# Performance work log

Hardware: AMD Instinct MI355X
Metric: run time of the kernel (lower is better)

Reference implementation:

```python
import jax, jax.numpy as jnp
import numpy as np

SIGMA = 4.0
KSIZE = 2 * int(4.0 * SIGMA + 0.5) + 1  # 33, as in anomalib's GaussianBlur2d
INPUT_SIZE = (224, 224)
NUM_NEIGHBORS = 9


def avg_pool_4_1_1(x):
    # nn.AvgPool2d(kernel_size=4, stride=1, padding=1), count_include_pad=True -> divide by 16
    s = jax.lax.reduce_window(x, 0.0, jax.lax.add, (1, 1, 4, 4), (1, 1, 1, 1),
                              ((0, 0), (0, 0), (1, 1), (1, 1)))
    return s / 16.0


def gaussian_kernel1d(ksize, sigma):
    x = jnp.arange(ksize, dtype=jnp.float32) - (ksize - 1) / 2.0
    g = jnp.exp(-0.5 * (x / sigma) ** 2)
    return g / jnp.sum(g)


def gaussian_blur(x):
    # separable 33x33 gaussian blur, reflect padding (kornia GaussianBlur2d default)
    k = gaussian_kernel1d(KSIZE, SIGMA)
    pad = KSIZE // 2
    xp = jnp.pad(x, ((0, 0), (0, 0), (pad, pad), (pad, pad)), mode='reflect')
    dn = ('NCHW', 'OIHW', 'NCHW')
    y = jax.lax.conv_general_dilated(xp, k.reshape(1, 1, KSIZE, 1), (1, 1), 'VALID', dimension_numbers=dn)
    y = jax.lax.conv_general_dilated(y, k.reshape(1, 1, 1, KSIZE), (1, 1), 'VALID', dimension_numbers=dn)
    return y


def euclidean_dist(x, y):
    # pairwise L2: x [..., n, d], y [..., m, d] -> [..., n, m]
    x2 = jnp.sum(x * x, axis=-1, keepdims=True)
    y2 = jnp.sum(y * y, axis=-1, keepdims=True)
    d2 = x2 - 2.0 * jnp.matmul(x, jnp.swapaxes(y, -1, -2)) + jnp.swapaxes(y2, -1, -2)
    return jnp.sqrt(jnp.clip(d2, 0.0, None))


def compute_anomaly_score(patch_scores, locations, embedding, memory_bank):
    # PatchCore re-weighting (num_neighbors > 1 branch)
    B, P = patch_scores.shape
    bidx = jnp.arange(B)
    max_patches = jnp.argmax(patch_scores, axis=1)                      # [B]
    feats = embedding.reshape(B, P, -1)[bidx, max_patches]              # [B, C]
    score = patch_scores[bidx, max_patches]                             # [B] s*
    nn_index = locations[bidx, max_patches]                             # [B]
    nn_sample = memory_bank[nn_index]                                   # [B, C]
    d_bank = euclidean_dist(nn_sample, memory_bank)                     # [B, M]
    _, support = jax.lax.top_k(-d_bank, NUM_NEIGHBORS)                  # [B, K] smallest
    support_feats = memory_bank[support]                                # [B, K, C]
    distances = euclidean_dist(feats[:, None, :], support_feats)        # [B, 1, K]
    weights = 1.0 - jnp.exp(score) / jnp.sum(jnp.exp(distances[:, 0, :]), axis=-1)
    return weights * score


def setup_inputs() -> dict:
    key = jax.random.key(0)
    k1, k2, k3 = jax.random.split(key, 3)
    feat_layer2 = jax.random.normal(k1, (8, 512, 28, 28), dtype=jnp.float32)
    feat_layer3 = jax.random.normal(k2, (8, 1024, 14, 14), dtype=jnp.float32)
    memory_bank = jax.random.normal(k3, (32000, 1536), dtype=jnp.float32)
    return {"feat_layer2": feat_layer2, "feat_layer3": feat_layer3, "memory_bank": memory_bank}


def reference(feat_layer2, feat_layer3, memory_bank):
    # feature_pooler = AvgPool2d(4,1,1)
    f2 = avg_pool_4_1_1(feat_layer2)   # [B, 512, 27, 27]
    f3 = avg_pool_4_1_1(feat_layer3)   # [B, 1024, 13, 13]
    B, _, H, W = f2.shape
    # generate_embedding: bilinear upsample layer3 to layer2 size, concat channels
    f3u = jax.image.resize(f3, (B, f3.shape[1], H, W), method='bilinear')
    emb = jnp.concatenate([f2, f3u], axis=1)                            # [B, 1536, 27, 27]
    C = emb.shape[1]
    embedding = jnp.transpose(emb, (0, 2, 3, 1)).reshape(-1, C)         # [B*H*W, C]
    # nearest_neighbors with n_neighbors=1 over the coreset memory bank
    d = euclidean_dist(embedding, memory_bank)                          # [B*H*W, M]
    patch_scores = jnp.min(d, axis=1).reshape(B, -1)
    locations = jnp.argmin(d, axis=1).reshape(B, -1)
    pred_score = compute_anomaly_score(patch_scores, locations, embedding, memory_bank)
    # anomaly map: upsample patch scores to input size + gaussian blur
    pmap = patch_scores.reshape(B, 1, H, W)
    amap = jax.image.resize(pmap, (B, 1, INPUT_SIZE[0], INPUT_SIZE[1]), method='bilinear')
    anomaly_map = gaussian_blur(amap)
    return anomaly_map, pred_score
```

## Files before the change

kernel.cpp:

```cpp
#include <hip/hip_runtime.h>
#include <math.h>

#define NB 8
#define C2 512
#define C3 1024
#define HIN2 28
#define HIN3 14
#define HO2 27
#define HO3 13
#define CC 1536
#define NP (NB*HO2*HO2)
#define NM 32000
#define NKNN 9
#define OH 224
#define AMAP_N (NB*OH*OH)

#define BM 256
#define BN 256
#define BK 64
#define KT (CC/BK)
#define MB_CNT ((NP+BM-1)/BM)
#define NB_CNT (NM/BN)
#define NWG (MB_CNT*NB_CNT)

typedef unsigned long long u64;
typedef unsigned int u32;
typedef __attribute__((ext_vector_type(8))) short bf16x8;
typedef __attribute__((ext_vector_type(4))) float f32x4;

struct GW { float w[33]; };

__device__ __forceinline__ float warp_sum(float v){
  #pragma unroll
  for (int off=32; off; off>>=1) v += __shfl_down(v, off);
  return v;
}

__device__ __forceinline__ ushort f2bf(float f){
  u32 u = __float_as_uint(f);
  u32 r = (u + 0x7FFFu + ((u>>16)&1u)) >> 16;
  return (ushort)r;
}
__device__ __forceinline__ float bf2f(ushort b){
  return __uint_as_float(((u32)b)<<16);
}

#define GLDS(g, l) __builtin_amdgcn_global_load_lds((const __attribute__((address_space(1))) void*)(g), (__attribute__((address_space(3))) void*)(l), 16, 0, 0)
#define WAITVM2() asm volatile("s_waitcnt vmcnt(2)" ::: "memory")
#define WAITVM0() asm volatile("s_waitcnt vmcnt(0)" ::: "memory")
__device__ __forceinline__ void bar_raw(){
  asm volatile("" ::: "memory");
  __builtin_amdgcn_s_barrier();
  asm volatile("" ::: "memory");
}

__global__ void k_avgpool2(const float* __restrict__ in, ushort* __restrict__ embB){
  int t = blockIdx.x*256 + threadIdx.x;
  if (t >= NB*HO2*HO2*C2) return;
  int c = t % C2; int r = t / C2;
  int j = r % HO2; r /= HO2;
  int i = r % HO2; int b = r / HO2;
  const float* plane = in + ((size_t)(b*C2 + c)*HIN2)*HIN2;
  float s = 0.f;
  #pragma unroll
  for (int di=0; di<4; ++di){
    int y = i - 1 + di;
    if ((unsigned)y >= HIN2) continue;
    #pragma unroll
    for (int dj=0; dj<4; ++dj){
      int x = j - 1 + dj;
      if ((unsigned)x < HIN2) s += plane[y*HIN2 + x];
    }
  }
  embB[((size_t)((b*HO2 + i)*HO2 + j))*CC + c] = f2bf(s * (1.f/16.f));
}

__global__ void k_avgpool3(const float* __restrict__ in, float* __restrict__ f3p){
  int t = blockIdx.x*256 + threadIdx.x;
  if (t >= NB*HO3*HO3*C3) return;
  int c = t % C3; int r = t / C3;
  int j = r % HO3; r /= HO3;
  int i = r % HO3; int b = r / HO3;
  const float* plane = in + ((size_t)(b*C3 + c)*HIN3)*HIN3;
  float s = 0.f;
  #pragma unroll
  for (int di=0; di<4; ++di){
    int y = i - 1 + di;
    if ((unsigned)y >= HIN3) continue;
    #pragma unroll
    for (int dj=0; dj<4; ++dj){
      int x = j - 1 + dj;
      if ((unsigned)x < HIN3) s += plane[y*HIN3 + x];
    }
  }
  f3p[((size_t)((b*HO3 + i)*HO3 + j))*C3 + c] = s * (1.f/16.f);
}

__global__ void k_upsample3(const float* __restrict__ f3p, ushort* __restrict__ embB){
  int t = blockIdx.x*256 + threadIdx.x;
  if (t >= NB*HO2*HO2*C3) return;
  int c = t % C3; int r = t / C3;
  int ox = r % HO2; r /= HO2;
  int oy = r % HO2; int b = r / HO2;
  float fy = (oy + 0.5f) * (13.f/27.f) - 0.5f;
  float fx = (ox + 0.5f) * (13.f/27.f) - 0.5f;
  int y0 = (int)floorf(fy); float wy = fy - (float)y0;
  int x0 = (int)floorf(fx); float wx = fx - (float)x0;
  int y0c = min(max(y0,0), HO3-1), y1c = min(max(y0+1,0), HO3-1);
  int x0c = min(max(x0,0), HO3-1), x1c = min(max(x0+1,0), HO3-1);
  const float* base = f3p + (size_t)(b*HO3*HO3)*C3;
  float v00 = base[(size_t)(y0c*HO3 + x0c)*C3 + c];
  float v01 = base[(size_t)(y0c*HO3 + x1c)*C3 + c];
  float v10 = base[(size_t)(y1c*HO3 + x0c)*C3 + c];
  float v11 = base[(size_t)(y1c*HO3 + x1c)*C3 + c];
  float v = (1.f-wy)*((1.f-wx)*v00 + wx*v01) + wy*((1.f-wx)*v10 + wx*v11);
  embB[((size_t)((b*HO2 + oy)*HO2 + ox))*CC + C2 + c] = f2bf(v);
}

__global__ void k_bank_prep(const float* __restrict__ bank, ushort* __restrict__ bankB,
                            float* __restrict__ y2){
  int wave = threadIdx.x >> 6, lane = threadIdx.x & 63;
  int r = blockIdx.x*4 + wave;
  if (r >= NM) return;
  const float4* p = (const float4*)(bank + (size_t)r*CC);
  ushort4* q = (ushort4*)(bankB + (size_t)r*CC);
  float s = 0.f;
  #pragma unroll
  for (int it=0; it<6; ++it){
    float4 v = p[it*64 + lane];
    s += v.x*v.x + v.y*v.y + v.z*v.z + v.w*v.w;
    ushort4 o; o.x = f2bf(v.x); o.y = f2bf(v.y); o.z = f2bf(v.z); o.w = f2bf(v.w);
    q[it*64 + lane] = o;
  }
  s = warp_sum(s);
  if (lane==0) y2[r] = s;
}

__global__ void k_rowsumsq_bf(const ushort* __restrict__ src, float* __restrict__ dst, int rows){
  int wave = threadIdx.x >> 6;
  int lane = threadIdx.x & 63;
  int r = blockIdx.x*4 + wave;
  if (r >= rows) return;
  const uint4* p = (const uint4*)(src + (size_t)r*CC);
  float s = 0.f;
  #pragma unroll
  for (int it=0; it<3; ++it){
    uint4 v = p[it*64 + lane];
    u32 ws_[4] = {v.x, v.y, v.z, v.w};
    #pragma unroll
    for (int q=0;q<4;q++){
      float lo = __uint_as_float(ws_[q]<<16);
      float hi = __uint_as_float(ws_[q]&0xFFFF0000u);
      s += lo*lo + hi*hi;
    }
  }
  s = warp_sum(s);
  if (lane==0) dst[r] = s;
}

__global__ void k_init(u64* __restrict__ packed){
  int t = blockIdx.x*256 + threadIdx.x;
  if (t < NP) packed[t] = ~0ull;
}

__global__ __launch_bounds__(512, 2) void k_distmin_mfma(
    const ushort* __restrict__ A, const ushort* __restrict__ B,
    const float* __restrict__ x2, const float* __restrict__ y2,
    u64* __restrict__ packed)
{
  __shared__ ushort smem[4*BM*BK];
  ushort* As0 = smem;
  ushort* Bs0 = smem + BM*BK;
  ushort* As1 = smem + 2*BM*BK;
  ushort* Bs1 = smem + 3*BM*BK;

  const int tid = threadIdx.x;
  const int w   = tid >> 6;
  const int l   = tid & 63;
  const int wr  = w >> 2;
  const int wc  = w & 3;
  const int ccol = l & 15;
  const int cgrp = l >> 4;

  int orig = blockIdx.x;
  const int q8 = NWG/8, r8 = NWG%8;
  int xcd = orig & 7, sidx = orig >> 3;
  int wg = (xcd < r8 ? xcd*(q8+1) : r8*(q8+1) + (xcd-r8)*q8) + sidx;
  const int mb = wg % MB_CNT;
  const int nb = wg / MB_CNT;
  const int m0 = mb * BM;
  const int n0 = nb * BN;

  const int rowin = l >> 3;
  const int scol  = (((l&7) ^ rowin) * 8);
  int chA1[2], chA2[2], chB1[2], chB2[2];
  u32 aO1[2], aO2[2], bO1[2], bO2[2];
  u32 lA1[2], lA2[2], lB1[2], lB2[2];
  #pragma unroll
  for (int c=0;c<2;c++){
    chA1[c] = (w<4) ? (2*w+c) : (8+2*w+c);
    chA2[c] = chA1[c] + 8;
    chB1[c] = (w>>1)*8 + (w&1)*2 + c;
    chB2[c] = chB1[c] + 4;
    aO1[c] = (u32)min(m0 + chA1[c]*8 + rowin, NP-1)*CC + scol;
    aO2[c] = (u32)min(m0 + chA2[c]*8 + rowin, NP-1)*CC + scol;
    bO1[c] = (u32)(n0 + chB1[c]*8 + rowin)*CC + scol;
    bO2[c] = (u32)(n0 + chB2[c]*8 + rowin)*CC + scol;
    lA1[c] = (u32)chA1[c]*1024 + l*16;
    lA2[c] = (u32)chA2[c]*1024 + l*16;
    lB1[c] = (u32)chB1[c]*1024 + l*16;
    lB2[c] = (u32)chB2[c]*1024 + l*16;
  }

  const u32 o0 = (u32)((cgrp ^ (ccol & 7)) * 8);
  u32 aRow[8], bRow[4];
  #pragma unroll
  for (int mi=0;mi<8;mi++) aRow[mi] = (u32)(wr*128 + mi*16 + ccol)*BK;
  #pragma unroll
  for (int ni=0;ni<4;ni++) bRow[ni] = (u32)(wc*64 + ni*16 + ccol)*BK;

  f32x4 acc[8][4];
  #pragma unroll
  for (int mi=0;mi<8;mi++)
    #pragma unroll
    for (int ni=0;ni<4;ni++)
      acc[mi][ni] = (f32x4){0.f,0.f,0.f,0.f};

  bf16x8 rAlo[4][2], rAhi[4][2], rBlo[2][2], rBhi[2][2];

  #pragma unroll
  for (int c=0;c<2;c++) GLDS(A + aO1[c], (char*)As0 + lA1[c]);
  #pragma unroll
  for (int c=0;c<2;c++) GLDS(B + bO1[c], (char*)Bs0 + lB1[c]);
  WAITVM0(); bar_raw();
  #pragma unroll
  for (int mi=0;mi<4;mi++)
    #pragma unroll
    for (int ks=0;ks<2;ks++)
      rAlo[mi][ks] = *(const bf16x8*)&As0[aRow[mi] + (o0 ^ (u32)(ks<<5))];
  #pragma unroll
  for (int ni=0;ni<2;ni++)
    #pragma unroll
    for (int ks=0;ks<2;ks++)
      rBlo[ni][ks] = *(const bf16x8*)&Bs0[bRow[ni] + (o0 ^ (u32)(ks<<5))];
  #pragma unroll
  for (int c=0;c<2;c++) GLDS(B + bO2[c], (char*)Bs0 + lB2[c]);
  #pragma unroll
  for (int c=0;c<2;c++) GLDS(A + aO2[c], (char*)As0 + lA2[c]);

  const ushort* cA = As0; const ushort* cB = Bs0;
  ushort* nA = As1; ushort* nB = Bs1;

  #pragma unroll 1
  for (int kt=0; kt<KT; ++kt){
    const u32 kk = (u32)(kt+1)*BK;

    WAITVM2(); bar_raw(); __builtin_amdgcn_sched_barrier(0);
    GLDS(A + aO1[0] + kk, (char*)nA + lA1[0]);
    GLDS(A + aO1[1] + kk, (char*)nA + lA1[1]);
    #pragma unroll
    for (int ni=0;ni<2;ni++)
      #pragma unroll
      for (int ks=0;ks<2;ks++)
        rBhi[ni][ks] = *(const bf16x8*)&cB[bRow[ni+2] + (o0 ^ (u32)(ks<<5))];
    __builtin_amdgcn_s_setprio(1);
    #pragma unroll
    for (int mi=0;mi<4;mi++)
      #pragma unroll
      for (int ni=0;ni<2;ni++)
        #pragma unroll
        for (int ks=0;ks<2;ks++)
          acc[mi][ni] = __builtin_amdgcn_mfma_f32_16x16x32_bf16(rAlo[mi][ks], rBlo[ni][ks], acc[mi][ni], 0, 0, 0);
    __builtin_amdgcn_s_setprio(0);

    WAITVM2(); bar_raw(); __builtin_amdgcn_sched_barrier(0);
    GLDS(B + bO1[0] + kk, (char*)nB + lB1[0]);
    GLDS(B + bO1[1] + kk, (char*)nB + lB1[1]);
    #pragma unroll
    for (int mi=0;mi<4;mi++)
      #pragma unroll
      for (int ks=0;ks<2;ks++)
        rAhi[mi][ks] = *(const bf16x8*)&cA[aRow[mi+4] + (o0 ^ (u32)(ks<<5))];
    __builtin_amdgcn_s_setprio(1);
    #pragma unroll
    for (int mi=0;mi<4;mi++)
      #pragma unroll
      for (int ni=0;ni<2;ni++)
        #pragma unroll
        for (int ks=0;ks<2;ks++)
          acc[mi][ni+2] = __builtin_amdgcn_mfma_f32_16x16x32_bf16(rAlo[mi][ks], rBhi[ni][ks], acc[mi][ni+2], 0, 0, 0);
    __builtin_amdgcn_s_setprio(0);

    WAITVM2(); bar_raw(); __builtin_amdgcn_sched_barrier(0);
    GLDS(B + bO2[0] + kk, (char*)nB + lB2[0]);
    GLDS(B + bO2[1] + kk, (char*)nB + lB2[1]);
    #pragma unroll
    for (int mi=0;mi<4;mi++)
      #pragma unroll
      for (int ks=0;ks<2;ks++)
        rAlo[mi][ks] = *(const bf16x8*)&((const ushort*)nA)[aRow[mi] + (o0 ^ (u32)(ks<<5))];
    __builtin_amdgcn_s_setprio(1);
    #pragma unroll
    for (int mi=0;mi<4;mi++)
      #pragma unroll
      for (int ni=0;ni<2;ni++)
        #pragma unroll
        for (int ks=0;ks<2;ks++)
          acc[mi+4][ni] = __builtin_amdgcn_mfma_f32_16x16x32_bf16(rAhi[mi][ks], rBlo[ni][ks], acc[mi+4][ni], 0, 0, 0);
    __builtin_amdgcn_s_setprio(0);

    WAITVM2(); bar_raw(); __builtin_amdgcn_sched_barrier(0);
    GLDS(A + aO2[0] + kk, (char*)nA + lA2[0]);
    GLDS(A + aO2[1] + kk, (char*)nA + lA2[1]);
    #pragma unroll
    for (int ni=0;ni<2;ni++)
      #pragma unroll
      for (int ks=0;ks<2;ks++)
        rBlo[ni][ks] = *(const bf16x8*)&((const ushort*)nB)[bRow[ni] + (o0 ^ (u32)(ks<<5))];
    __builtin_amdgcn_s_setprio(1);
    #pragma unroll
    for (int mi=0;mi<4;mi++)
      #pragma unroll
      for (int ni=0;ni<2;ni++)
        #pragma unroll
        for (int ks=0;ks<2;ks++)
          acc[mi+4][ni+2] = __builtin_amdgcn_mfma_f32_16x16x32_bf16(rAhi[mi][ks], rBhi[ni][ks], acc[mi+4][ni+2], 0, 0, 0);
    __builtin_amdgcn_s_setprio(0);

    ushort* t1 = (ushort*)cA; cA = nA; nA = t1;
    ushort* t2 = (ushort*)cB; cB = nB; nB = t2;
  }
  WAITVM0();

  float xv[8][4];
  #pragma unroll
  for (int mi=0;mi<8;mi++)
    #pragma unroll
    for (int r=0;r<4;r++)
      xv[mi][r] = x2[min(m0 + wr*128 + mi*16 + cgrp*4 + r, NP-1)];

  u64 best[8][4];
  #pragma unroll
  for (int mi=0;mi<8;mi++)
    #pragma unroll
    for (int r=0;r<4;r++) best[mi][r] = ~0ull;

  #pragma unroll
  for (int ni=0;ni<4;ni++){
    const int n = n0 + wc*64 + ni*16 + ccol;
    const float yy = y2[n];
    #pragma unroll
    for (int mi=0;mi<8;mi++)
      #pragma unroll
      for (int r=0;r<4;r++){
        float d2 = fmaxf(xv[mi][r] + yy - 2.f*acc[mi][ni][r], 0.f);
        u64 pk = (((u64)__float_as_uint(d2))<<32) | (u32)n;
        if (pk < best[mi][r]) best[mi][r] = pk;
      }
  }

  #pragma unroll
  for (int mi=0;mi<8;mi++)
    #pragma unroll
    for (int r=0;r<4;r++){
      u64 pk = best[mi][r];
      #pragma unroll
      for (int md=1; md<16; md<<=1){
        u64 o = __shfl_xor(pk, md);
        if (o < pk) pk = o;
      }
      const int row = m0 + wr*128 + mi*16 + cgrp*4 + r;
      if (ccol==0 && row < NP) atomicMin(&packed[row], pk);
    }
}

__global__ void k_unpack(const u64* __restrict__ packed, float* __restrict__ patch_d, int* __restrict__ loc){
  int t = blockIdx.x*256 + threadIdx.x;
  if (t < NP){
    u64 v = packed[t];
    patch_d[t] = sqrtf(__uint_as_float((u32)(v>>32)));
    loc[t] = (int)(v & 0xffffffffu);
  }
}

__global__ void k_argmax(const float* __restrict__ patch_d, const int* __restrict__ loc,
                         int* __restrict__ sel_mp, float* __restrict__ sel_score, int* __restrict__ sel_nn){
  int b = blockIdx.x;
  int tid = threadIdx.x;
  __shared__ u64 red[4];
  u64 best = 0;
  for (int p = tid; p < HO2*HO2; p += 256){
    float v = patch_d[b*HO2*HO2 + p];
    u64 pk = (((u64)__float_as_uint(v))<<32) | (u32)(HO2*HO2 - p);
    if (pk > best) best = pk;
  }
  int lane = tid & 63, w = tid >> 6;
  #pragma unroll
  for (int d=32; d; d>>=1){ u64 o = __shfl_down(best, d); if (o > best) best = o; }
  if (lane==0) red[w] = best;
  __syncthreads();
  if (tid==0){
    u64 bb = red[0];
    for (int q=1;q<4;q++) if (red[q] > bb) bb = red[q];
    int p = HO2*HO2 - (int)(bb & 0xffffffffu);
    sel_mp[b] = p;
    sel_score[b] = __uint_as_float((u32)(bb>>32));
    sel_nn[b] = loc[b*HO2*HO2 + p];
  }
}

__device__ __forceinline__ void bf8dec(uint4 v, float* f){
  u32 a[4] = {v.x, v.y, v.z, v.w};
  #pragma unroll
  for (int q=0;q<4;q++){
    f[2*q]   = __uint_as_float(a[q]<<16);
    f[2*q+1] = __uint_as_float(a[q]&0xFFFF0000u);
  }
}

__global__ __launch_bounds__(256) void k_dbank(const ushort* __restrict__ bankB, const float* __restrict__ y2,
    const int* __restrict__ sel_nn, float* __restrict__ d_bank){
  int wave = threadIdx.x >> 6, lane = threadIdx.x & 63;
  int m = blockIdx.x*4 + wave;
  if (m >= NM) return;
  int nn[NB];
  #pragma unroll
  for (int b=0;b<NB;b++) nn[b] = sel_nn[b];
  const uint4* pm = (const uint4*)(bankB + (size_t)m*CC);
  float acc[NB];
  #pragma unroll
  for (int b=0;b<NB;b++) acc[b] = 0.f;
  #pragma unroll
  for (int it=0; it<3; ++it){
    uint4 v = pm[it*64 + lane];
    float vf[8]; bf8dec(v, vf);
    #pragma unroll
    for (int b=0;b<NB;b++){
      uint4 u = ((const uint4*)(bankB + (size_t)nn[b]*CC))[it*64 + lane];
      float uf[8]; bf8dec(u, uf);
      #pragma unroll
      for (int q=0;q<8;q++) acc[b] += vf[q]*uf[q];
    }
  }
  #pragma unroll
  for (int b=0;b<NB;b++){
    float s = warp_sum(acc[b]);
    if (lane==0) d_bank[(size_t)b*NM + m] = fmaxf(y2[nn[b]] + y2[m] - 2.f*s, 0.f);
  }
}

__global__ __launch_bounds__(256) void k_score(const float* __restrict__ d_bank, const float* __restrict__ bank,
    const ushort* __restrict__ embB, const float* __restrict__ x2, const float* __restrict__ y2,
    const int* __restrict__ sel_mp, const float* __restrict__ sel_score, float* __restrict__ out_score){
  int b = blockIdx.x, tid = threadIdx.x;
  __shared__ u64 cand[256*NKNN];
  __shared__ int sel[NKNN];
  __shared__ u64 red[4];
  __shared__ u64 gbest_s;
  __shared__ float fred[4];
  __shared__ float sumexp_s;

  #pragma unroll
  for (int q=0;q<NKNN;q++) cand[tid*NKNN+q] = ~0ull;
  for (int m = tid; m < NM; m += 256){
    float v = d_bank[(size_t)b*NM + m];
    u64 pk = (((u64)__float_as_uint(v))<<32) | (u32)m;
    if (pk < cand[tid*NKNN + NKNN-1]){
      cand[tid*NKNN + NKNN-1] = pk;
      for (int q=NKNN-1; q>0 && cand[tid*NKNN+q] < cand[tid*NKNN+q-1]; --q){
        u64 t = cand[tid*NKNN+q]; cand[tid*NKNN+q] = cand[tid*NKNN+q-1]; cand[tid*NKNN+q-1] = t;
      }
    }
  }
  __syncthreads();
  int lane = tid & 63, w = tid >> 6;
  for (int k=0;k<NKNN;++k){
    u64 mybest = ~0ull;
    #pragma unroll
    for (int q=0;q<NKNN;q++){ u64 v = cand[tid*NKNN+q]; if (v < mybest) mybest = v; }
    u64 rb = mybest;
    #pragma unroll
    for (int d=32; d; d>>=1){ u64 o = __shfl_down(rb, d); if (o < rb) rb = o; }
    if (lane==0) red[w] = rb;
    __syncthreads();
    if (tid==0){
      u64 bb = red[0];
      for (int q=1;q<4;q++) if (red[q] < bb) bb = red[q];
      gbest_s = bb;
      sel[k] = (int)(bb & 0xffffffffu);
    }
    __syncthreads();
    u64 gb = gbest_s;
    #pragma unroll
    for (int q=0;q<NKNN;q++) if (cand[tid*NKNN+q] == gb) cand[tid*NKNN+q] = ~0ull;
    __syncthreads();
  }

  int mp = sel_mp[b];
  const ushort* fv = embB + (size_t)(b*HO2*HO2 + mp)*CC;
  float fx2 = x2[b*HO2*HO2 + mp];
  if (tid==0) sumexp_s = 0.f;
  __syncthreads();
  for (int k=0;k<NKNN;++k){
    const float* sv = bank + (size_t)sel[k]*CC;
    float part = 0.f;
    for (int i = tid; i < CC; i += 256) part += bf2f(fv[i])*sv[i];
    part = warp_sum(part);
    if (lane==0) fred[w] = part;
    __syncthreads();
    if (tid==0){
      float dot = fred[0]+fred[1]+fred[2]+fred[3];
      float d2 = fmaxf(fx2 + y2[sel[k]] - 2.f*dot, 0.f);
      sumexp_s += expf(sqrtf(d2));
    }
    __syncthreads();
  }
  if (tid==0){
    float s = sel_score[b];
    out_score[b] = (1.f - expf(s)/sumexp_s) * s;
  }
}

__global__ void k_amap_bilinear(const float* __restrict__ patch_d, float* __restrict__ amap){
  int t = blockIdx.x*256 + threadIdx.x;
  if (t >= AMAP_N) return;
  int x = t % OH; int r = t / OH;
  int y = r % OH; int b = r / OH;
  float fy = (y + 0.5f) * (27.f/224.f) - 0.5f;
  float fx = (x + 0.5f) * (27.f/224.f) - 0.5f;
  int y0 = (int)floorf(fy); float wy = fy - (float)y0;
  int x0 = (int)floorf(fx); float wx = fx - (float)x0;
  int y0c = min(max(y0,0),HO2-1), y1c = min(max(y0+1,0),HO2-1);
  int x0c = min(max(x0,0),HO2-1), x1c = min(max(x0+1,0),HO2-1);
  const float* p = patch_d + b*HO2*HO2;
  float v = (1.f-wy)*((1.f-wx)*p[y0c*HO2+x0c] + wx*p[y0c*HO2+x1c])
          + wy*((1.f-wx)*p[y1c*HO2+x0c] + wx*p[y1c*HO2+x1c]);
  amap[t] = v;
}

__global__ void k_blur_h(const float* __restrict__ in, float* __restrict__ out, GW gw){
  int t = blockIdx.x*256 + threadIdx.x;
  if (t >= AMAP_N) return;
  int x = t % OH; int rest = t / OH;
  const float* row = in + (size_t)rest*OH;
  float s = 0.f;
  #pragma unroll
  for (int k=0;k<33;++k){
    int xx = x + k - 16;
    xx = (xx < 0) ? -xx : xx;
    xx = (xx > OH-1) ? (2*(OH-1) - xx) : xx;
    s += gw.w[k]*row[xx];
  }
  out[t] = s;
}

__global__ void k_blur_v(const float* __restrict__ in, float* __restrict__ out, GW gw){
  int t = blockIdx.x*256 + threadIdx.x;
  if (t >= AMAP_N) return;
  int x = t % OH; int r = t / OH;
  int y = r % OH; int b = r / OH;
  const float* img = in + (size_t)b*OH*OH;
  float s = 0.f;
  #pragma unroll
  for (int k=0;k<33;++k){
    int yy = y + k - 16;
    yy = (yy < 0) ? -yy : yy;
    yy = (yy > OH-1) ? (2*(OH-1) - yy) : yy;
    s += gw.w[k]*img[(size_t)yy*OH + x];
  }
  out[t] = s;
}

extern "C" void kernel_launch(void* const* d_in, const int* in_sizes, int n_in,
                              void* d_out, int out_size, void* d_ws, size_t ws_size,
                              hipStream_t stream){
  const float* f2   = (const float*)d_in[0];
  const float* f3   = (const float*)d_in[1];
  const float* bank = (const float*)d_in[2];
  float* out = (float*)d_out;

  char* ws = (char*)d_ws;
  size_t off = 0;
  auto alloc = [&](size_t bytes)->char*{ char* p = ws + off; off += (bytes + 255) & ~(size_t)255; return p; };
  ushort* embB    = (ushort*)alloc((size_t)NP*CC*2);
  ushort* bankB   = (ushort*)alloc((size_t)NM*CC*2);
  float* f3p      = (float*)alloc((size_t)NB*HO3*HO3*C3*4);
  float* y2       = (float*)alloc((size_t)NM*4);
  float* x2       = (float*)alloc((size_t)NP*4);
  u64*   packed   = (u64*)  alloc((size_t)NP*8);
  float* patch_d  = (float*)alloc((size_t)NP*4);
  int*   loc      = (int*)  alloc((size_t)NP*4);
  float* d_bank   = (float*)alloc((size_t)NB*NM*4);
  int*   sel_mp   = (int*)  alloc(NB*4);
  float* sel_scr  = (float*)alloc(NB*4);
  int*   sel_nn   = (int*)  alloc(NB*4);
  float* amap1    = (float*)alloc((size_t)AMAP_N*4);
  float* amap2    = (float*)alloc((size_t)AMAP_N*4);

  GW gw;
  { float s=0.f; for(int i=0;i<33;i++){ float xx=(float)i-16.f; gw.w[i]=expf(-0.5f*(xx/4.f)*(xx/4.f)); s+=gw.w[i]; }
    for(int i=0;i<33;i++) gw.w[i]/=s; }

  k_avgpool2<<<(NB*HO2*HO2*C2+255)/256,256,0,stream>>>(f2, embB);
  k_avgpool3<<<(NB*HO3*HO3*C3+255)/256,256,0,stream>>>(f3, f3p);
  k_upsample3<<<(NB*HO2*HO2*C3+255)/256,256,0,stream>>>(f3p, embB);
  k_bank_prep<<<(NM+3)/4,256,0,stream>>>(bank, bankB, y2);
  k_rowsumsq_bf<<<(NP+3)/4,256,0,stream>>>(embB, x2, NP);
  k_init<<<(NP+255)/256,256,0,stream>>>(packed);
  k_distmin_mfma<<<NWG,512,0,stream>>>(embB, bankB, x2, y2, packed);
  k_unpack<<<(NP+255)/256,256,0,stream>>>(packed, patch_d, loc);
  k_argmax<<<NB,256,0,stream>>>(patch_d, loc, sel_mp, sel_scr, sel_nn);
  k_dbank<<<(NM+3)/4,256,0,stream>>>(bankB, y2, sel_nn, d_bank);
  k_score<<<NB,256,0,stream>>>(d_bank, bank, embB, x2, y2, sel_mp, sel_scr, out + AMAP_N);
  k_amap_bilinear<<<(AMAP_N+255)/256,256,0,stream>>>(patch_d, amap1);
  k_blur_h<<<(AMAP_N+255)/256,256,0,stream>>>(amap1, amap2, gw);
  k_blur_v<<<(AMAP_N+255)/256,256,0,stream>>>(amap2, out, gw);
}
```

Measured before the change: 1.041 ms.

## Restructure GEMM pipeline, stage avgpool in LDS, fuse upsample+blur as matrix

Reworks the MFMA distance-min main loop so each quarter reads its LDS fragments from the current buffer right before use, with vmcnt(4) waits and extra barriers, instead of prefetching from the next buffer. The avgpool kernels now stage per-channel planes in shared memory with coalesced float4 loads, and the packed-init is folded into the row-norm kernel. The bilinear upsample and separable reflect blur are folded into one precomputed 224x27 operator applied as two small matmuls per image in a single kernel. k_score moves to 512 threads. The extra barriers in the GEMM could add stalls, and the fused anomaly-map kernel runs only 8 blocks.

```diff
diff --git a/kernel.cpp b/kernel.cpp
--- a/kernel.cpp
+++ b/kernel.cpp
@@ -46,54 +46,74 @@
 }
 
 #define GLDS(g, l) __builtin_amdgcn_global_load_lds((const __attribute__((address_space(1))) void*)(g), (__attribute__((address_space(3))) void*)(l), 16, 0, 0)
-#define WAITVM2() asm volatile("s_waitcnt vmcnt(2)" ::: "memory")
+#define WAITVM4() asm volatile("s_waitcnt vmcnt(4)" ::: "memory")
 #define WAITVM0() asm volatile("s_waitcnt vmcnt(0)" ::: "memory")
+#define WAITLGKM0() asm volatile("s_waitcnt lgkmcnt(0)" ::: "memory")
+#define SB0() __builtin_amdgcn_sched_barrier(0)
 __device__ __forceinline__ void bar_raw(){
   asm volatile("" ::: "memory");
   __builtin_amdgcn_s_barrier();
   asm volatile("" ::: "memory");
 }
 
-__global__ void k_avgpool2(const float* __restrict__ in, ushort* __restrict__ embB){
-  int t = blockIdx.x*256 + threadIdx.x;
-  if (t >= NB*HO2*HO2*C2) return;
-  int c = t % C2; int r = t / C2;
-  int j = r % HO2; r /= HO2;
-  int i = r % HO2; int b = r / HO2;
-  const float* plane = in + ((size_t)(b*C2 + c)*HIN2)*HIN2;
-  float s = 0.f;
-  #pragma unroll
-  for (int di=0; di<4; ++di){
-    int y = i - 1 + di;
-    if ((unsigned)y >= HIN2) continue;
-    #pragma unroll
-    for (int dj=0; dj<4; ++dj){
-      int x = j - 1 + dj;
-      if ((unsigned)x < HIN2) s += plane[y*HIN2 + x];
-    }
-  }
-  embB[((size_t)((b*HO2 + i)*HO2 + j))*CC + c] = f2bf(s * (1.f/16.f));
-}
-
-__global__ void k_avgpool3(const float* __restrict__ in, float* __restrict__ f3p){
-  int t = blockIdx.x*256 + threadIdx.x;
-  if (t >= NB*HO3*HO3*C3) return;
-  int c = t % C3; int r = t / C3;
-  int j = r % HO3; r /= HO3;
-  int i = r % HO3; int b = r / HO3;
-  const float* plane = in + ((size_t)(b*C3 + c)*HIN3)*HIN3;
-  float s = 0.f;
-  #pragma unroll
-  for (int di=0; di<4; ++di){
-    int y = i - 1 + di;
-    if ((unsigned)y >= HIN3) continue;
-    #pragma unroll
-    for (int dj=0; dj<4; ++dj){
-      int x = j - 1 + dj;
-      if ((unsigned)x < HIN3) s += plane[y*HIN3 + x];
-    }
-  }
-  f3p[((size_t)((b*HO3 + i)*HO3 + j))*C3 + c] = s * (1.f/16.f);
+__global__ __launch_bounds__(256) void k_avgpool2(const float* __restrict__ in, ushort* __restrict__ embB){
+  __shared__ float pl[16*789];
+  int b = blockIdx.x >> 5, cg = blockIdx.x & 31;
+  const float4* src = (const float4*)(in + ((size_t)b*C2 + cg*16)*(HIN2*HIN2));
+  for (int idx = threadIdx.x; idx < 16*196; idx += 256){
+    int c = idx/196, p4 = idx - c*196;
+    float4 v = src[idx];
+    float* d = &pl[c*789 + p4*4];
+    d[0]=v.x; d[1]=v.y; d[2]=v.z; d[3]=v.w;
+  }
+  __syncthreads();
+  int c = threadIdx.x & 15, g = threadIdx.x >> 4;
+  for (int pos = g; pos < HO2*HO2; pos += 16){
+    int i = pos/HO2, j = pos - i*HO2;
+    const float* p = &pl[c*789];
+    float s = 0.f;
+    #pragma unroll
+    for (int di=0; di<4; ++di){
+      int y = i - 1 + di;
+      if ((unsigned)y >= HIN2) continue;
+      #pragma unroll
+      for (int dj=0; dj<4; ++dj){
+        int x = j - 1 + dj;
+        if ((unsigned)x < HIN2) s += p[y*HIN2 + x];
+      }
+    }
+    embB[((size_t)((b*HO2 + i)*HO2 + j))*CC + cg*16 + c] = f2bf(s * (1.f/16.f));
+  }
+}
+
+__global__ __launch_bounds__(256) void k_avgpool3(const float* __restrict__ in, float* __restrict__ f3p){
+  __shared__ float pl[64*197];
+  int b = blockIdx.x >> 4, cg = blockIdx.x & 15;
+  const float4* src = (const float4*)(in + ((size_t)b*C3 + cg*64)*(HIN3*HIN3));
+  for (int idx = threadIdx.x; idx < 64*49; idx += 256){
+    int c = idx/49, p4 = idx - c*49;
+    float4 v = src[idx];
+    float* d = &pl[c*197 + p4*4];
+    d[0]=v.x; d[1]=v.y; d[2]=v.z; d[3]=v.w;
+  }
+  __syncthreads();
+  int c = threadIdx.x & 63, g = threadIdx.x >> 6;
+  for (int pos = g; pos < HO3*HO3; pos += 4){
+    int i = pos/HO3, j = pos - i*HO3;
+    const float* p = &pl[c*197];
+    float s = 0.f;
+    #pragma unroll
+    for (int di=0; di<4; ++di){
+      int y = i - 1 + di;
+      if ((unsigned)y >= HIN3) continue;
+      #pragma unroll
+      for (int dj=0; dj<4; ++dj){
+        int x = j - 1 + dj;
+        if ((unsigned)x < HIN3) s += p[y*HIN3 + x];
+      }
+    }
+    f3p[((size_t)((b*HO3 + i)*HO3 + j))*C3 + cg*64 + c] = s * (1.f/16.f);
+  }
 }
 
 __global__ void k_upsample3(const float* __restrict__ f3p, ushort* __restrict__ embB){
@@ -136,7 +156,8 @@
   if (lane==0) y2[r] = s;
 }
 
-__global__ void k_rowsumsq_bf(const ushort* __restrict__ src, float* __restrict__ dst, int rows){
+__global__ void k_rowsumsq_bf(const ushort* __restrict__ src, float* __restrict__ dst, int rows,
+                              u64* __restrict__ packed){
   int wave = threadIdx.x >> 6;
   int lane = threadIdx.x & 63;
   int r = blockIdx.x*4 + wave;
@@ -155,12 +176,7 @@
     }
   }
   s = warp_sum(s);
-  if (lane==0) dst[r] = s;
-}
-
-__global__ void k_init(u64* __restrict__ packed){
-  int t = blockIdx.x*256 + threadIdx.x;
-  if (t < NP) packed[t] = ~0ull;
+  if (lane==0){ dst[r] = s; packed[r] = ~0ull; }
 }
 
 __global__ __launch_bounds__(512, 2) void k_distmin_mfma(
@@ -228,25 +244,16 @@
 
   bf16x8 rAlo[4][2], rAhi[4][2], rBlo[2][2], rBhi[2][2];
 
-  #pragma unroll
-  for (int c=0;c<2;c++) GLDS(A + aO1[c], (char*)As0 + lA1[c]);
-  #pragma unroll
-  for (int c=0;c<2;c++) GLDS(B + bO1[c], (char*)Bs0 + lB1[c]);
-  WAITVM0(); bar_raw();
-  #pragma unroll
-  for (int mi=0;mi<4;mi++)
-    #pragma unroll
-    for (int ks=0;ks<2;ks++)
-      rAlo[mi][ks] = *(const bf16x8*)&As0[aRow[mi] + (o0 ^ (u32)(ks<<5))];
-  #pragma unroll
-  for (int ni=0;ni<2;ni++)
-    #pragma unroll
-    for (int ks=0;ks<2;ks++)
-      rBlo[ni][ks] = *(const bf16x8*)&Bs0[bRow[ni] + (o0 ^ (u32)(ks<<5))];
-  #pragma unroll
-  for (int c=0;c<2;c++) GLDS(B + bO2[c], (char*)Bs0 + lB2[c]);
-  #pragma unroll
-  for (int c=0;c<2;c++) GLDS(A + aO2[c], (char*)As0 + lA2[c]);
+  GLDS(A + aO1[0], (char*)As0 + lA1[0]);
+  GLDS(A + aO1[1], (char*)As0 + lA1[1]);
+  GLDS(B + bO1[0], (char*)Bs0 + lB1[0]);
+  GLDS(B + bO1[1], (char*)Bs0 + lB1[1]);
+  GLDS(B + bO2[0], (char*)Bs0 + lB2[0]);
+  GLDS(B + bO2[1], (char*)Bs0 + lB2[1]);
+  GLDS(A + aO2[0], (char*)As0 + lA2[0]);
+  GLDS(A + aO2[1], (char*)As0 + lA2[1]);
+  WAITVM4();
+  bar_raw();
 
   const ushort* cA = As0; const ushort* cB = Bs0;
   ushort* nA = As1; ushort* nB = Bs1;
@@ -255,14 +262,19 @@
   for (int kt=0; kt<KT; ++kt){
     const u32 kk = (u32)(kt+1)*BK;
 
-    WAITVM2(); bar_raw(); __builtin_amdgcn_sched_barrier(0);
+    #pragma unroll
+    for (int mi=0;mi<4;mi++)
+      #pragma unroll
+      for (int ks=0;ks<2;ks++)
+        rAlo[mi][ks] = *(const bf16x8*)&cA[aRow[mi] + (o0 ^ (u32)(ks<<5))];
+    #pragma unroll
+    for (int ni=0;ni<2;ni++)
+      #pragma unroll
+      for (int ks=0;ks<2;ks++)
+        rBlo[ni][ks] = *(const bf16x8*)&cB[bRow[ni] + (o0 ^ (u32)(ks<<5))];
     GLDS(A + aO1[0] + kk, (char*)nA + lA1[0]);
     GLDS(A + aO1[1] + kk, (char*)nA + lA1[1]);
-    #pragma unroll
-    for (int ni=0;ni<2;ni++)
-      #pragma unroll
-      for (int ks=0;ks<2;ks++)
-        rBhi[ni][ks] = *(const bf16x8*)&cB[bRow[ni+2] + (o0 ^ (u32)(ks<<5))];
+    bar_raw(); WAITLGKM0(); SB0();
     __builtin_amdgcn_s_setprio(1);
     #pragma unroll
     for (int mi=0;mi<4;mi++)
@@ -272,15 +284,17 @@
         for (int ks=0;ks<2;ks++)
           acc[mi][ni] = __builtin_amdgcn_mfma_f32_16x16x32_bf16(rAlo[mi][ks], rBlo[ni][ks], acc[mi][ni], 0, 0, 0);
     __builtin_amdgcn_s_setprio(0);
-
-    WAITVM2(); bar_raw(); __builtin_amdgcn_sched_barrier(0);
+    WAITVM4();
+    bar_raw();
+
+    #pragma unroll
+    for (int ni=0;ni<2;ni++)
+      #pragma unroll
+      for (int ks=0;ks<2;ks++)
+        rBhi[ni][ks] = *(const bf16x8*)&cB[bRow[ni+2] + (o0 ^ (u32)(ks<<5))];
     GLDS(B + bO1[0] + kk, (char*)nB + lB1[0]);
     GLDS(B + bO1[1] + kk, (char*)nB + lB1[1]);
-    #pragma unroll
-    for (int mi=0;mi<4;mi++)
-      #pragma unroll
-      for (int ks=0;ks<2;ks++)
-        rAhi[mi][ks] = *(const bf16x8*)&cA[aRow[mi+4] + (o0 ^ (u32)(ks<<5))];
+    bar_raw(); WAITLGKM0(); SB0();
     __builtin_amdgcn_s_setprio(1);
     #pragma unroll
     for (int mi=0;mi<4;mi++)
@@ -290,15 +304,17 @@
         for (int ks=0;ks<2;ks++)
           acc[mi][ni+2] = __builtin_amdgcn_mfma_f32_16x16x32_bf16(rAlo[mi][ks], rBhi[ni][ks], acc[mi][ni+2], 0, 0, 0);
     __builtin_amdgcn_s_setprio(0);
-
-    WAITVM2(); bar_raw(); __builtin_amdgcn_sched_barrier(0);
+    WAITVM4();
+    bar_raw();
+
+    #pragma unroll
+    for (int mi=0;mi<4;mi++)
+      #pragma unroll
+      for (int ks=0;ks<2;ks++)
+        rAhi[mi][ks] = *(const bf16x8*)&cA[aRow[mi+4] + (o0 ^ (u32)(ks<<5))];
     GLDS(B + bO2[0] + kk, (char*)nB + lB2[0]);
     GLDS(B + bO2[1] + kk, (char*)nB + lB2[1]);
-    #pragma unroll
-    for (int mi=0;mi<4;mi++)
-      #pragma unroll
-      for (int ks=0;ks<2;ks++)
-        rAlo[mi][ks] = *(const bf16x8*)&((const ushort*)nA)[aRow[mi] + (o0 ^ (u32)(ks<<5))];
+    bar_raw(); WAITLGKM0(); SB0();
     __builtin_amdgcn_s_setprio(1);
     #pragma unroll
     for (int mi=0;mi<4;mi++)
@@ -308,15 +324,11 @@
         for (int ks=0;ks<2;ks++)
           acc[mi+4][ni] = __builtin_amdgcn_mfma_f32_16x16x32_bf16(rAhi[mi][ks], rBlo[ni][ks], acc[mi+4][ni], 0, 0, 0);
     __builtin_amdgcn_s_setprio(0);
-
-    WAITVM2(); bar_raw(); __builtin_amdgcn_sched_barrier(0);
+    bar_raw();
+
     GLDS(A + aO2[0] + kk, (char*)nA + lA2[0]);
     GLDS(A + aO2[1] + kk, (char*)nA + lA2[1]);
-    #pragma unroll
-    for (int ni=0;ni<2;ni++)
-      #pragma unroll
-      for (int ks=0;ks<2;ks++)
-        rBlo[ni][ks] = *(const bf16x8*)&((const ushort*)nB)[bRow[ni] + (o0 ^ (u32)(ks<<5))];
+    bar_raw();
     __builtin_amdgcn_s_setprio(1);
     #pragma unroll
     for (int mi=0;mi<4;mi++)
@@ -326,6 +338,8 @@
         for (int ks=0;ks<2;ks++)
           acc[mi+4][ni+2] = __builtin_amdgcn_mfma_f32_16x16x32_bf16(rAhi[mi][ks], rBhi[ni][ks], acc[mi+4][ni+2], 0, 0, 0);
     __builtin_amdgcn_s_setprio(0);
+    WAITVM4();
+    bar_raw();
 
     ushort* t1 = (ushort*)cA; cA = nA; nA = t1;
     ushort* t2 = (ushort*)cB; cB = nB; nB = t2;
@@ -449,20 +463,20 @@
   }
 }
 
-__global__ __launch_bounds__(256) void k_score(const float* __restrict__ d_bank, const float* __restrict__ bank,
+__global__ __launch_bounds__(512) void k_score(const float* __restrict__ d_bank, const float* __restrict__ bank,
     const ushort* __restrict__ embB, const float* __restrict__ x2, const float* __restrict__ y2,
     const int* __restrict__ sel_mp, const float* __restrict__ sel_score, float* __restrict__ out_score){
   int b = blockIdx.x, tid = threadIdx.x;
-  __shared__ u64 cand[256*NKNN];
+  __shared__ u64 cand[512*NKNN];
   __shared__ int sel[NKNN];
-  __shared__ u64 red[4];
+  __shared__ u64 red[8];
   __shared__ u64 gbest_s;
-  __shared__ float fred[4];
+  __shared__ float fred[8];
   __shared__ float sumexp_s;
 
   #pragma unroll
   for (int q=0;q<NKNN;q++) cand[tid*NKNN+q] = ~0ull;
-  for (int m = tid; m < NM; m += 256){
+  for (int m = tid; m < NM; m += 512){
     float v = d_bank[(size_t)b*NM + m];
     u64 pk = (((u64)__float_as_uint(v))<<32) | (u32)m;
     if (pk < cand[tid*NKNN + NKNN-1]){
@@ -485,7 +499,7 @@
     __syncthreads();
     if (tid==0){
       u64 bb = red[0];
-      for (int q=1;q<4;q++) if (red[q] < bb) bb = red[q];
+      for (int q=1;q<8;q++) if (red[q] < bb) bb = red[q];
       gbest_s = bb;
       sel[k] = (int)(bb & 0xffffffffu);
     }
@@ -504,12 +518,13 @@
   for (int k=0;k<NKNN;++k){
     const float* sv = bank + (size_t)sel[k]*CC;
     float part = 0.f;
-    for (int i = tid; i < CC; i += 256) part += bf2f(fv[i])*sv[i];
+    for (int i = tid; i < CC; i += 512) part += bf2f(fv[i])*sv[i];
     part = warp_sum(part);
     if (lane==0) fred[w] = part;
     __syncthreads();
     if (tid==0){
-      float dot = fred[0]+fred[1]+fred[2]+fred[3];
+      float dot = 0.f;
+      for (int q=0;q<8;q++) dot += fred[q];
       float d2 = fmaxf(fx2 + y2[sel[k]] - 2.f*dot, 0.f);
       sumexp_s += expf(sqrtf(d2));
     }
@@ -521,54 +536,49 @@
   }
 }
 
-__global__ void k_amap_bilinear(const float* __restrict__ patch_d, float* __restrict__ amap){
-  int t = blockIdx.x*256 + threadIdx.x;
-  if (t >= AMAP_N) return;
-  int x = t % OH; int r = t / OH;
-  int y = r % OH; int b = r / OH;
-  float fy = (y + 0.5f) * (27.f/224.f) - 0.5f;
-  float fx = (x + 0.5f) * (27.f/224.f) - 0.5f;
-  int y0 = (int)floorf(fy); float wy = fy - (float)y0;
-  int x0 = (int)floorf(fx); float wx = fx - (float)x0;
-  int y0c = min(max(y0,0),HO2-1), y1c = min(max(y0+1,0),HO2-1);
-  int x0c = min(max(x0,0),HO2-1), x1c = min(max(x0+1,0),HO2-1);
-  const float* p = patch_d + b*HO2*HO2;
-  float v = (1.f-wy)*((1.f-wx)*p[y0c*HO2+x0c] + wx*p[y0c*HO2+x1c])
-          + wy*((1.f-wx)*p[y1c*HO2+x0c] + wx*p[y1c*HO2+x1c]);
-  amap[t] = v;
-}
-
-__global__ void k_blur_h(const float* __restrict__ in, float* __restrict__ out, GW gw){
-  int t = blockIdx.x*256 + threadIdx.x;
-  if (t >= AMAP_N) return;
-  int x = t % OH; int rest = t / OH;
-  const float* row = in + (size_t)rest*OH;
+__global__ void k_maketab(float* __restrict__ T, GW gw){
+  int idx = blockIdx.x*256 + threadIdx.x;
+  if (idx >= OH*HO2) return;
+  int x = idx / HO2, j = idx - x*HO2;
   float s = 0.f;
   #pragma unroll
   for (int k=0;k<33;++k){
-    int xx = x + k - 16;
-    xx = (xx < 0) ? -xx : xx;
-    xx = (xx > OH-1) ? (2*(OH-1) - xx) : xx;
-    s += gw.w[k]*row[xx];
-  }
-  out[t] = s;
-}
-
-__global__ void k_blur_v(const float* __restrict__ in, float* __restrict__ out, GW gw){
-  int t = blockIdx.x*256 + threadIdx.x;
-  if (t >= AMAP_N) return;
-  int x = t % OH; int r = t / OH;
-  int y = r % OH; int b = r / OH;
-  const float* img = in + (size_t)b*OH*OH;
-  float s = 0.f;
-  #pragma unroll
-  for (int k=0;k<33;++k){
-    int yy = y + k - 16;
+    int yy = x + k - 16;
     yy = (yy < 0) ? -yy : yy;
     yy = (yy > OH-1) ? (2*(OH-1) - yy) : yy;
-    s += gw.w[k]*img[(size_t)yy*OH + x];
-  }
-  out[t] = s;
+    float fy = (yy + 0.5f) * (27.f/224.f) - 0.5f;
+    int y0 = (int)floorf(fy); float wy = fy - (float)y0;
+    int j0 = min(max(y0,0), HO2-1), j1 = min(max(y0+1,0), HO2-1);
+    float c = ((j==j0)?(1.f-wy):0.f) + ((j==j1)?wy:0.f);
+    s += gw.w[k]*c;
+  }
+  T[idx] = s;
+}
+
+__global__ __launch_bounds__(256) void k_amap_fused(const float* __restrict__ patch_d,
+    const float* __restrict__ T, float* __restrict__ out){
+  __shared__ float Ts[OH*HO2];
+  __shared__ float ps[HO2*HO2];
+  __shared__ float tmp[HO2*OH];
+  int b = blockIdx.x, t = threadIdx.x;
+  for (int idx=t; idx<OH*HO2; idx+=256) Ts[idx] = T[idx];
+  for (int idx=t; idx<HO2*HO2; idx+=256) ps[idx] = patch_d[b*HO2*HO2+idx];
+  __syncthreads();
+  for (int idx=t; idx<HO2*OH; idx+=256){
+    int i = idx/OH, x = idx - i*OH;
+    float s = 0.f;
+    #pragma unroll
+    for (int j=0;j<HO2;j++) s += ps[i*HO2+j]*Ts[x*HO2+j];
+    tmp[i*OH+x] = s;
+  }
+  __syncthreads();
+  for (int idx=t; idx<OH*OH; idx+=256){
+    int y = idx/OH, x = idx - y*OH;
+    float s = 0.f;
+    #pragma unroll
+    for (int i=0;i<HO2;i++) s += Ts[y*HO2+i]*tmp[i*OH+x];
+    out[(size_t)b*OH*OH + idx] = s;
+  }
 }
 
 extern "C" void kernel_launch(void* const* d_in, const int* in_sizes, int n_in,
@@ -594,25 +604,22 @@
   int*   sel_mp   = (int*)  alloc(NB*4);
   float* sel_scr  = (float*)alloc(NB*4);
   int*   sel_nn   = (int*)  alloc(NB*4);
-  float* amap1    = (float*)alloc((size_t)AMAP_N*4);
-  float* amap2    = (float*)alloc((size_t)AMAP_N*4);
+  float* Tmat     = (float*)alloc((size_t)OH*HO2*4);
 
   GW gw;
   { float s=0.f; for(int i=0;i<33;i++){ float xx=(float)i-16.f; gw.w[i]=expf(-0.5f*(xx/4.f)*(xx/4.f)); s+=gw.w[i]; }
     for(int i=0;i<33;i++) gw.w[i]/=s; }
 
-  k_avgpool2<<<(NB*HO2*HO2*C2+255)/256,256,0,stream>>>(f2, embB);
-  k_avgpool3<<<(NB*HO3*HO3*C3+255)/256,256,0,stream>>>(f3, f3p);
+  k_avgpool2<<<NB*32,256,0,stream>>>(f2, embB);
+  k_avgpool3<<<NB*16,256,0,stream>>>(f3, f3p);
   k_upsample3<<<(NB*HO2*HO2*C3+255)/256,256,0,stream>>>(f3p, embB);
   k_bank_prep<<<(NM+3)/4,256,0,stream>>>(bank, bankB, y2);
-  k_rowsumsq_bf<<<(NP+3)/4,256,0,stream>>>(embB, x2, NP);
-  k_init<<<(NP+255)/256,256,0,stream>>>(packed);
+  k_rowsumsq_bf<<<(NP+3)/4,256,0,stream>>>(embB, x2, NP, packed);
+  k_maketab<<<(OH*HO2+255)/256,256,0,stream>>>(Tmat, gw);
   k_distmin_mfma<<<NWG,512,0,stream>>>(embB, bankB, x2, y2, packed);
   k_unpack<<<(NP+255)/256,256,0,stream>>>(packed, patch_d, loc);
   k_argmax<<<NB,256,0,stream>>>(patch_d, loc, sel_mp, sel_scr, sel_nn);
   k_dbank<<<(NM+3)/4,256,0,stream>>>(bankB, y2, sel_nn, d_bank);
-  k_score<<<NB,256,0,stream>>>(d_bank, bank, embB, x2, y2, sel_mp, sel_scr, out + AMAP_N);
-  k_amap_bilinear<<<(AMAP_N+255)/256,256,0,stream>>>(patch_d, amap1);
-  k_blur_h<<<(AMAP_N+255)/256,256,0,stream>>>(amap1, amap2, gw);
-  k_blur_v<<<(AMAP_N+255)/256,256,0,stream>>>(amap2, out, gw);
-}
+  k_score<<<NB,512,0,stream>>>(d_bank, bank, embB, x2, y2, sel_mp, sel_scr, out + AMAP_N);
+  k_amap_fused<<<NB,256,0,stream>>>(patch_d, Tmat, out);
+}
```

After: 949.6 us. -8.8%, faster.
